# Kernel optimization log

Hardware: AMD Instinct MI355X
Metric: run time of the kernel (lower is better)

## Reference

```python
import jax, jax.numpy as jnp
import numpy as np

B, S, D, H, DH = 2, 4096, 768, 12, 64
L = 2                      # encoder layers (reduced-depth longformer-base)
HW = 256                   # one-sided sliding window (attention_window = 512)
C = 2 * HW                 # query chunk size
NC = S // C                # number of chunks
KW = C + 2 * HW            # key-window length per chunk
V = 50265
SEP_ID, NSEP = 2, 32       # </s> token id; SEPs per block (fixed by construction)
G = NSEP + 1               # global tokens: <s> at pos 0 + all SEPs
NCLS = 5
EPS = 1e-5
NEG = -1e9


def layer_norm(x, gb):
    m = jnp.mean(x, -1, keepdims=True)
    v = jnp.var(x, -1, keepdims=True)
    return (x - m) * jax.lax.rsqrt(v + EPS) * gb[0] + gb[1]


def split_heads(x):  # [B,S,D] -> [B,H,S,DH]
    return x.reshape(B, S, H, DH).transpose(0, 2, 1, 3)


def window_gather(x):  # [B,H,S,DH] -> [B,H,NC,KW,DH] overlapping key windows
    xp = jnp.pad(x, ((0, 0), (0, 0), (HW, HW), (0, 0)))
    idx = (jnp.arange(NC) * C)[:, None] + jnp.arange(KW)[None, :]
    return xp[:, :, idx, :]


def longformer_attn(x, amask, gpos, wqkv, bqkv, wqkv_g, bqkv_g, wo, bo):
    q = split_heads(x @ wqkv[0] + bqkv[0]) / np.float32(np.sqrt(DH))
    k = split_heads(x @ wqkv[1] + bqkv[1])
    v = split_heads(x @ wqkv[2] + bqkv[2])

    # ----- local sliding-window scores (banded, chunked) -----
    kw = window_gather(k)
    vw = window_gather(v)
    qc = q.reshape(B, H, NC, C, DH)
    s_loc = jnp.einsum('bhncd,bhnkd->bhnck', qc, kw)  # [B,H,NC,C,KW]

    rel = jnp.arange(KW)[None, :] - jnp.arange(C)[:, None]          # [C,KW]
    band_ok = (rel >= 0) & (rel <= 2 * HW)
    key_pos = (jnp.arange(NC) * C)[:, None] + jnp.arange(KW)[None, :] - HW
    in_b = (key_pos >= 0) & (key_pos < S)                            # [NC,KW]
    amp = jnp.pad(amask, ((0, 0), (HW, HW)))
    idx = (jnp.arange(NC) * C)[:, None] + jnp.arange(KW)[None, :]
    am_w = amp[:, idx] > 0                                           # [B,NC,KW]
    mask = band_ok[None, None, None] & in_b[None, None, :, None, :] & am_w[:, None, :, None, :]
    s_loc = jnp.where(mask, s_loc, NEG).reshape(B, H, S, KW)

    # ----- scores of every query against the G global keys -----
    gidx = gpos[:, None, :, None]                                    # [B,1,G,1]
    kg = jnp.take_along_axis(k, gidx, axis=2)                        # [B,H,G,DH]
    vg = jnp.take_along_axis(v, gidx, axis=2)
    s_glob = jnp.einsum('bhsd,bhgd->bhsg', q, kg)                    # [B,H,S,G]

    probs = jax.nn.softmax(jnp.concatenate([s_glob, s_loc], -1), -1)
    pg, pl = probs[..., :G], probs[..., G:]
    ctx = jnp.einsum('bhsg,bhgd->bhsd', pg, vg)
    ctx = ctx + jnp.einsum('bhnck,bhnkd->bhncd', pl.reshape(B, H, NC, C, KW), vw).reshape(B, H, S, DH)

    # ----- global tokens attend to everything (separate projections) -----
    qg = split_heads(x @ wqkv_g[0] + bqkv_g[0]) / np.float32(np.sqrt(DH))
    kgf = split_heads(x @ wqkv_g[1] + bqkv_g[1])
    vgf = split_heads(x @ wqkv_g[2] + bqkv_g[2])
    qg = jnp.take_along_axis(qg, gidx, axis=2)                       # [B,H,G,DH]
    s_g = jnp.einsum('bhgd,bhsd->bhgs', qg, kgf)                     # [B,H,G,S]
    s_g = jnp.where(amask[:, None, None, :] > 0, s_g, NEG)
    og = jnp.einsum('bhgs,bhsd->bhgd', jax.nn.softmax(s_g, -1), vgf)

    ctx_m = ctx.transpose(0, 2, 1, 3).reshape(B, S, D)
    og_m = og.transpose(0, 2, 1, 3).reshape(B, G, D)
    ctx_m = ctx_m.at[jnp.arange(B)[:, None], gpos].set(og_m)         # replace global rows
    return ctx_m @ wo + bo


def setup_inputs() -> dict:
    key = jax.random.key(0)
    ks = jax.random.split(key, 12)
    ids = jax.random.randint(ks[0], (B, S), 5, V, dtype=jnp.int32)
    sep_positions = (jnp.arange(NSEP) + 1) * (S // NSEP) - 1         # SEP every 128 toks
    ids = ids.at[:, sep_positions].set(SEP_ID).at[:, 0].set(0)       # <s> at pos 0
    att = jnp.ones((B, S), jnp.int32)

    def nrm(k, shp):
        return jax.random.normal(k, shp, jnp.float32) * 0.02

    ln = jnp.stack([jnp.ones(D, jnp.float32), jnp.zeros(D, jnp.float32)])
    return dict(
        input_ids=ids, attention_mask=att,
        word_emb=nrm(ks[1], (V, D)), pos_emb=nrm(ks[2], (S + 2, D)),
        type_emb=nrm(ks[3], (D,)), emb_ln=ln,
        Wqkv=nrm(ks[4], (L, 3, D, D)), bqkv=jnp.zeros((L, 3, D), jnp.float32),
        Wqkv_g=nrm(ks[5], (L, 3, D, D)), bqkv_g=jnp.zeros((L, 3, D), jnp.float32),
        Wo=nrm(ks[6], (L, D, D)), bo=jnp.zeros((L, D), jnp.float32),
        ln1=jnp.broadcast_to(ln, (L, 2, D)),
        Wff1=nrm(ks[7], (L, D, 4 * D)), bff1=jnp.zeros((L, 4 * D), jnp.float32),
        Wff2=nrm(ks[8], (L, 4 * D, D)), bff2=jnp.zeros((L, D), jnp.float32),
        ln2=jnp.broadcast_to(ln, (L, 2, D)),
        cls_W=nrm(ks[9], (NCLS, D)), cls_b=jnp.zeros((NCLS,), jnp.float32),
    )


def reference(input_ids, attention_mask, word_emb, pos_emb, type_emb, emb_ln,
              Wqkv, bqkv, Wqkv_g, bqkv_g, Wo, bo, ln1, Wff1, bff1, Wff2, bff2,
              ln2, cls_W, cls_b):
    # global attention mask: pos 0 + every SEP (fixed count by construction)
    sep_pos = jnp.sort(jnp.where(input_ids == SEP_ID, jnp.arange(S)[None, :], S), -1)[:, :NSEP]
    sep_pos = sep_pos.astype(jnp.int32)
    gpos = jnp.concatenate([jnp.zeros((B, 1), jnp.int32), sep_pos], 1)  # [B,G]

    x = word_emb[input_ids] + pos_emb[jnp.arange(S) + 2][None] + type_emb
    x = layer_norm(x, emb_ln)
    for l in range(L):
        a = longformer_attn(x, attention_mask, gpos, Wqkv[l], bqkv[l],
                            Wqkv_g[l], bqkv_g[l], Wo[l], bo[l])
        x = layer_norm(x + a, ln1[l])
        f = jax.nn.gelu(x @ Wff1[l] + bff1[l], approximate=False) @ Wff2[l] + bff2[l]
        x = layer_norm(x + f, ln2[l])

    # gather SEP embeddings (row-major over batch then sentence) -> classifier
    h = jnp.take_along_axis(x, sep_pos[:, :, None], axis=1).reshape(B * NSEP, D)
    return h @ cls_W.T + cls_b
```

## Files before the change

kernel.cpp:

```cpp
#include <hip/hip_runtime.h>


#define Bb 2
#define Ss 4096
#define Dd 768
#define Hh 12
#define Gg 33
#define NSEPn 32
#define Ll 2
#define SPAD 4640
#define PADL 256
#define NCLSn 5
#define NCH 16
#define PARTF 1056
#define PSTR 72

typedef unsigned short u16;
typedef __attribute__((ext_vector_type(8))) short bv8;
typedef __attribute__((ext_vector_type(4))) short sv4;
typedef __attribute__((ext_vector_type(4))) float f32x4;

__device__ __forceinline__ float bf2f(u16 u) {
  unsigned v = ((unsigned)u) << 16;
  return __builtin_bit_cast(float, v);
}
__device__ __forceinline__ u16 f2bf(float f) {
  unsigned u = __builtin_bit_cast(unsigned, f);
  u += 0x7fffu + ((u >> 16) & 1u);
  return (u16)(u >> 16);
}
__device__ __forceinline__ void glds16(const void* g, void* l) {
  __builtin_amdgcn_global_load_lds(
      (const __attribute__((address_space(1))) void*)g,
      (__attribute__((address_space(3))) void*)l, 16, 0, 0);
}

__global__ __launch_bounds__(256)
void setup_kernel(int* __restrict__ cnt, u16* __restrict__ kpk,
                  u16* __restrict__ vtpk, const float* __restrict__ bqkv,
                  const float* __restrict__ bqkvg, float* __restrict__ biasc) {
  int tid = blockIdx.x * 256 + threadIdx.x;
  if (tid < Bb) cnt[tid] = 0;
  if (tid < Ll * 3840) {
    int l = tid / 3840, c = tid - l * 3840;
    float v = (c < 2304) ? bqkv[l * 2304 + c]
                         : bqkvg[(l * 3 + 1) * Dd + (c - 2304)];
    biasc[tid] = v;
  }
  const int PADW = SPAD - Ss;
  const int total = Bb * Hh * PADW * 64;
  for (int i = tid; i < total; i += gridDim.x * 256) {
    int bh = i / (PADW * 64);
    int rem = i - bh * (PADW * 64);
    int prow = rem >> 6, d = rem & 63;
    int row = (prow < PADL) ? prow : (Ss + prow);
    kpk[((size_t)bh * SPAD + row) * 64 + d] = 0;
    vtpk[((size_t)bh * 64 + d) * SPAD + row] = 0;
  }
}

__global__ void sep_find_kernel(const int* __restrict__ ids, int* __restrict__ cnt,
                                int* __restrict__ list) {
  int i = blockIdx.x * 256 + threadIdx.x;
  if (i >= Bb * Ss) return;
  int b = i >> 12;
  if (ids[i] == 2) {
    int idx = atomicAdd(&cnt[b], 1);
    if (idx < 64) list[b * 64 + idx] = i & (Ss - 1);
  }
}

__global__ void sep_sort_kernel(const int* __restrict__ cnt, const int* __restrict__ list,
                                int* __restrict__ gpos) {
  int b = blockIdx.x;
  int t = threadIdx.x;
  int n = cnt[b]; if (n > 64) n = 64;
  if (t < Gg) gpos[b * Gg + t] = (t == 0) ? 0 : (Ss - 1);
  __syncthreads();
  if (t < n) {
    int v = list[b * 64 + t];
    int rank = 0;
    for (int j = 0; j < n; ++j) rank += (list[b * 64 + j] < v) ? 1 : 0;
    if (rank < NSEPn) gpos[b * Gg + 1 + rank] = v;
  }
}

__global__ __launch_bounds__(256)
void wconv_kernel(const float* __restrict__ src0, u16* __restrict__ dst0,
                  int K, int N, int grp, int sstr, long unit, long WLs) {
  __shared__ float t[32][33];
  int z = blockIdx.z;
  const float* src = src0 + (size_t)((z / grp) * sstr + (z % grp)) * K * N;
  u16* dst = dst0 + (size_t)(z / grp) * WLs + (size_t)(z % grp) * unit;
  int n0 = blockIdx.x * 32, k0 = blockIdx.y * 32;
  int tx = threadIdx.x & 31, ty = threadIdx.x >> 5;
  #pragma unroll
  for (int i = 0; i < 4; ++i)
    t[ty + i * 8][tx] = src[(size_t)(k0 + ty + i * 8) * N + n0 + tx];
  __syncthreads();
  #pragma unroll
  for (int i = 0; i < 4; ++i)
    dst[(size_t)(n0 + ty + i * 8) * K + k0 + tx] = f2bf(t[tx][ty + i * 8]);
}

__global__ __launch_bounds__(256)
void embed_ln_kernel(const int* __restrict__ ids, const float* __restrict__ we,
                     const float* __restrict__ pe, const float* __restrict__ te,
                     const float* __restrict__ lnp, float* __restrict__ x,
                     u16* __restrict__ xb) {
  int row = blockIdx.x;
  int s = row & (Ss - 1);
  int id = ids[row];
  int tid = threadIdx.x;
  float v[3]; float sm = 0.f, s2 = 0.f;
  #pragma unroll
  for (int i = 0; i < 3; ++i) {
    int c = tid + i * 256;
    float t = we[(size_t)id * Dd + c] + pe[(size_t)(s + 2) * Dd + c] + te[c];
    v[i] = t; sm += t; s2 += t * t;
  }
  __shared__ float r1[256], r2[256];
  r1[tid] = sm; r2[tid] = s2; __syncthreads();
  for (int o = 128; o; o >>= 1) {
    if (tid < o) { r1[tid] += r1[tid + o]; r2[tid] += r2[tid + o]; }
    __syncthreads();
  }
  float mean = r1[0] * (1.f / 768.f);
  float var  = r2[0] * (1.f / 768.f) - mean * mean;
  float rs = rsqrtf(var + 1e-5f);
  #pragma unroll
  for (int i = 0; i < 3; ++i) {
    int c = tid + i * 256;
    float o = (v[i] - mean) * rs * lnp[c] + lnp[Dd + c];
    x[(size_t)row * Dd + c] = o;
    xb[(size_t)row * Dd + c] = f2bf(o);
  }
}

__global__ __launch_bounds__(256)
void add_ln3_kernel(const float* __restrict__ xin, const float* __restrict__ y0,
                    const u16* __restrict__ y1, const float* __restrict__ lnp,
                    float* __restrict__ xout, u16* __restrict__ xbout) {
  int row = blockIdx.x;
  int tid = threadIdx.x;
  float v[3]; float sm = 0.f, s2 = 0.f;
  #pragma unroll
  for (int i = 0; i < 3; ++i) {
    int c = tid + i * 256;
    size_t idx = (size_t)row * Dd + c;
    float t = xin[idx] + y0[idx] + bf2f(y1[idx]);
    v[i] = t; sm += t; s2 += t * t;
  }
  __shared__ float r1[256], r2[256];
  r1[tid] = sm; r2[tid] = s2; __syncthreads();
  for (int o = 128; o; o >>= 1) {
    if (tid < o) { r1[tid] += r1[tid + o]; r2[tid] += r2[tid + o]; }
    __syncthreads();
  }
  float mean = r1[0] * (1.f / 768.f);
  float var  = r2[0] * (1.f / 768.f) - mean * mean;
  float rs = rsqrtf(var + 1e-5f);
  #pragma unroll
  for (int i = 0; i < 3; ++i) {
    int c = tid + i * 256;
    float o = (v[i] - mean) * rs * lnp[c] + lnp[Dd + c];
    xout[(size_t)row * Dd + c] = o;
    xbout[(size_t)row * Dd + c] = f2bf(o);
  }
}

template <int MODE, bool XSWZ>
__global__ __launch_bounds__(256)
void gemm2_kernel(const u16* __restrict__ A, const u16* __restrict__ Bt,
                  const float* __restrict__ bias, float* __restrict__ outf,
                  u16* __restrict__ o0, u16* __restrict__ o1, u16* __restrict__ o2,
                  u16* __restrict__ o3, u16* __restrict__ o4,
                  int N, int Ks, int Kl, float scale) {
  __shared__ u16 la[2][128 * 32], lb[2][128 * 32];
  int tid = threadIdx.x;
  int wave = tid >> 6, lane = tid & 63;
  int wr = wave >> 1, wc = wave & 1;
  int lg = lane >> 4, lc = lane & 15;
  int bx = blockIdx.x, by = blockIdx.y;
  if (XSWZ) {
    int gx = gridDim.x;
    int nlin = bx + gx * by;
    int NB = gx * gridDim.y;
    nlin = (nlin & 7) * (NB >> 3) + (nlin >> 3);
    bx = nlin % gx;
    by = nlin / gx;
  }
  int row0 = by * 128, col0 = bx * 128;
  int koff = blockIdx.z * Kl;

  int sgr = (lane & 3) ^ ((lane >> 3) & 3);
  const u16* Ag = A + (size_t)(row0 + wave * 32 + (lane >> 2)) * Ks + sgr * 8 + koff;
  const u16* Bg = Bt + (size_t)(col0 + wave * 32 + (lane >> 2)) * Ks + sgr * 8 + koff;
  int wofs = wave * 1024;
  int gph = (lg ^ ((lc >> 1) & 3)) * 8;

  f32x4 acc[4][4];
  #pragma unroll
  for (int m = 0; m < 4; ++m)
    #pragma unroll
    for (int n = 0; n < 4; ++n) acc[m][n] = (f32x4){0.f, 0.f, 0.f, 0.f};

  glds16(Ag, la[0] + wofs);
  glds16(Ag + (size_t)16 * Ks, la[0] + wofs + 512);
  glds16(Bg, lb[0] + wofs);
  glds16(Bg + (size_t)16 * Ks, lb[0] + wofs + 512);
  __syncthreads();

  int nk = Kl >> 5;
  for (int t = 0; t < nk; ++t) {
    int cur = t & 1;
    if (t + 1 < nk) {
      int k1 = (t + 1) << 5;
      glds16(Ag + k1, la[cur ^ 1] + wofs);
      glds16(Ag + (size_t)16 * Ks + k1, la[cur ^ 1] + wofs + 512);
      glds16(Bg + k1, lb[cur ^ 1] + wofs);
      glds16(Bg + (size_t)16 * Ks + k1, lb[cur ^ 1] + wofs + 512);
    }
    bv8 af[4], bf_[4];
    #pragma unroll
    for (int m = 0; m < 4; ++m)
      af[m] = *reinterpret_cast<const bv8*>(la[cur] + (wr * 64 + m * 16 + lc) * 32 + gph);
    #pragma unroll
    for (int n = 0; n < 4; ++n)
      bf_[n] = *reinterpret_cast<const bv8*>(lb[cur] + (wc * 64 + n * 16 + lc) * 32 + gph);
    __builtin_amdgcn_s_setprio(1);
    #pragma unroll
    for (int m = 0; m < 4; ++m)
      #pragma unroll
      for (int n = 0; n < 4; ++n)
        acc[m][n] = __builtin_amdgcn_mfma_f32_16x16x32_bf16(af[m], bf_[n], acc[m][n], 0, 0, 0);
    __builtin_amdgcn_s_setprio(0);
    __syncthreads();
  }

  #pragma unroll
  for (int m = 0; m < 4; ++m) {
    int grow0 = row0 + wr * 64 + m * 16 + lg * 4;
    #pragma unroll
    for (int n = 0; n < 4; ++n) {
      int gcol = col0 + wc * 64 + n * 16 + lc;
      float bvl = bias[gcol];
      if (MODE == 0) {
        if (blockIdx.z == 0) {
          #pragma unroll
          for (int r = 0; r < 4; ++r)
            outf[(size_t)(grow0 + r) * N + gcol] = acc[m][n][r] + bvl;
        } else {
          #pragma unroll
          for (int r = 0; r < 4; ++r)
            o0[(size_t)(grow0 + r) * N + gcol] = f2bf(acc[m][n][r]);
        }
      } else if (MODE == 1) {
        #pragma unroll
        for (int r = 0; r < 4; ++r) {
          float v = acc[m][n][r] + bvl;
          v = 0.5f * v * (1.0f + erff(v * 0.70710678118654752f));
          o0[(size_t)(grow0 + r) * N + gcol] = f2bf(v);
        }
      } else if (MODE == 4) {
        #pragma unroll
        for (int r = 0; r < 4; ++r)
          o0[(size_t)(grow0 + r) * N + gcol] = f2bf((acc[m][n][r] + bvl) * scale);
      } else if (MODE == 2) {
        int sec = (col0 >> 7) / 6;
        int colr = gcol - sec * 768;
        int hh = colr >> 6, d = colr & 63;
        int bb = grow0 >> 12, s = grow0 & (Ss - 1);
        size_t bhh = (size_t)(bb * Hh + hh);
        if (sec == 0) {
          #pragma unroll
          for (int r = 0; r < 4; ++r)
            o0[(bhh * Ss + s + r) * 64 + d] = f2bf((acc[m][n][r] + bvl) * scale);
        } else if (sec == 1) {
          #pragma unroll
          for (int r = 0; r < 4; ++r)
            o1[(bhh * SPAD + PADL + s + r) * 64 + d] = f2bf(acc[m][n][r] + bvl);
        } else if (sec == 2) {
          sv4 pk;
          #pragma unroll
          for (int r = 0; r < 4; ++r) pk[r] = (short)f2bf(acc[m][n][r] + bvl);
          *reinterpret_cast<sv4*>(o2 + (bhh * 64 + d) * SPAD + PADL + s) = pk;
        } else if (sec == 3) {
          #pragma unroll
          for (int r = 0; r < 4; ++r)
            o3[(bhh * Ss + s + r) * 64 + d] = f2bf(acc[m][n][r] + bvl);
        } else {
          sv4 pk;
          #pragma unroll
          for (int r = 0; r < 4; ++r) pk[r] = (short)f2bf(acc[m][n][r] + bvl);
          *reinterpret_cast<sv4*>(o4 + (bhh * 64 + d) * Ss + s) = pk;
        }
      }
    }
  }
}

__global__ __launch_bounds__(256)
void gather_glob_kernel(const u16* __restrict__ kpk, const u16* __restrict__ vtpk,
                        const int* __restrict__ gpos, u16* __restrict__ kg,
                        u16* __restrict__ vgt) {
  int bh = blockIdx.x;
  int b = bh / Hh;
  int tid = threadIdx.x;
  for (int idx = tid; idx < 64 * 64; idx += 256) {
    int g = idx >> 6, d = idx & 63;
    u16 kv = 0, vv = 0;
    if (g < Gg) {
      int p = gpos[b * Gg + g];
      kv = kpk[((size_t)bh * SPAD + PADL + p) * 64 + d];
      vv = vtpk[((size_t)bh * 64 + d) * SPAD + PADL + p];
    }
    kg[(size_t)bh * 4096 + idx] = kv;
    vgt[((size_t)bh * 64 + d) * 64 + g] = vv;
  }
}

__global__ __launch_bounds__(256)
void gather_xg_kernel(const u16* __restrict__ xb, const int* __restrict__ gpos,
                      u16* __restrict__ xg) {
  int rg = blockIdx.x;
  int b = rg / Gg;
  int p = gpos[rg];
  int tid = threadIdx.x;
  for (int c = tid; c < Dd; c += 256)
    xg[(size_t)rg * Dd + c] = xb[((size_t)b * Ss + p) * Dd + c];
}

#define LOCAL_NB (Bb * Hh * (Ss / 64))
__global__ __launch_bounds__(128)
void attn_local_kernel(const u16* __restrict__ qpk, const u16* __restrict__ kpk,
                       const u16* __restrict__ vtpk, const u16* __restrict__ kg,
                       const u16* __restrict__ vgt, const int* __restrict__ amask,
                       u16* __restrict__ ctx) {
  __shared__ u16 Plds[4][16 * PSTR];
  int bid = blockIdx.x;
  int swz = (bid & 7) * (LOCAL_NB / 8) + (bid >> 3);
  int qb = swz & 63;
  int bh = swz >> 6;
  int b = bh / Hh;
  int h = bh - b * Hh;
  int wv = threadIdx.x >> 6;
  int q0 = qb * 64;
  int qA = q0 + wv * 32;
  int lane = threadIdx.x & 63;
  int lg = lane >> 4, lc = lane & 15;
  int lg4 = lg * 4;
  int qa = qA + lc, qbq = qA + 16 + lc;

  const u16* qrowA = qpk + ((size_t)bh * Ss + qA + lc) * 64;
  bv8 aqA0 = *reinterpret_cast<const bv8*>(qrowA + lg * 8);
  bv8 aqA1 = *reinterpret_cast<const bv8*>(qrowA + 32 + lg * 8);
  const u16* qrowB = qrowA + 16 * 64;
  bv8 aqB0 = *reinterpret_cast<const bv8*>(qrowB + lg * 8);
  bv8 aqB1 = *reinterpret_cast<const bv8*>(qrowB + 32 + lg * 8);

  f32x4 oA[4], oB[4];
  #pragma unroll
  for (int i = 0; i < 4; ++i) { oA[i] = (f32x4){0.f,0.f,0.f,0.f}; oB[i] = (f32x4){0.f,0.f,0.f,0.f}; }
  float mrunA = -1e30f, lrunA = 0.f, mrunB = -1e30f, lrunB = 0.f;

  const u16* kgb = kg + ((size_t)bh) * 64 * 64;
  const u16* vgb = vgt + ((size_t)bh) * 64 * 64;
  const u16* kb = kpk + ((size_t)bh) * SPAD * 64;
  const u16* vb = vtpk + ((size_t)bh) * 64 * SPAD;
  const int* amb = amask + b * Ss;
  u16* PA = &Plds[wv * 2][0];
  u16* PB = &Plds[wv * 2 + 1][0];

  bv8 kc[8];
  #pragma unroll
  for (int j = 0; j < 4; ++j) {
    const u16* kr = kgb + (size_t)(j * 16 + lc) * 64;
    kc[2 * j]     = *reinterpret_cast<const bv8*>(kr + lg * 8);
    kc[2 * j + 1] = *reinterpret_cast<const bv8*>(kr + 32 + lg * 8);
  }
  int amvN;
  { int ni = min(max(q0 - 256 + lane, 0), Ss - 1); amvN = amb[ni]; }

  for (int step = 0; step < 10; ++step) {
    bool isg = (step == 0);
    int ks = isg ? 0 : (q0 - 256 + (step - 1) * 64);
    int amvC = amvN;
    if (step < 9) { int ni = min(max(q0 - 256 + step * 64 + lane, 0), Ss - 1); amvN = amb[ni]; }

    bv8 vf0[4], vf1[4];
    #pragma unroll
    for (int nt = 0; nt < 4; ++nt) {
      const u16* vr = isg ? (vgb + (size_t)(nt * 16 + lc) * 64)
                          : (vb + (size_t)(nt * 16 + lc) * SPAD + PADL + ks);
      vf0[nt] = *reinterpret_cast<const bv8*>(vr + lg * 8);
      vf1[nt] = *reinterpret_cast<const bv8*>(vr + 32 + lg * 8);
    }
    unsigned long long kmask;
    if (isg) {
      kmask = (1ull << Gg) - 1;
    } else {
      int kidx = ks + lane;
      kmask = __ballot((kidx >= 0) && (kidx < Ss) && (amvC > 0));
    }
    f32x4 scA[4], scB[4];
    __builtin_amdgcn_s_setprio(1);
    #pragma unroll
    for (int j = 0; j < 4; ++j) {
      f32x4 z = (f32x4){0.f, 0.f, 0.f, 0.f};
      scA[j] = __builtin_amdgcn_mfma_f32_16x16x32_bf16(kc[2 * j], aqA0, z, 0, 0, 0);
      scA[j] = __builtin_amdgcn_mfma_f32_16x16x32_bf16(kc[2 * j + 1], aqA1, scA[j], 0, 0, 0);
      scB[j] = __builtin_amdgcn_mfma_f32_16x16x32_bf16(kc[2 * j], aqB0, z, 0, 0, 0);
      scB[j] = __builtin_amdgcn_mfma_f32_16x16x32_bf16(kc[2 * j + 1], aqB1, scB[j], 0, 0, 0);
    }
    __builtin_amdgcn_s_setprio(0);
    if (step < 9) {
      int ksn = q0 - 256 + step * 64;
      #pragma unroll
      for (int j = 0; j < 4; ++j) {
        const u16* kr = kb + (size_t)(PADL + ksn + j * 16 + lc) * 64;
        kc[2 * j]     = *reinterpret_cast<const bv8*>(kr + lg * 8);
        kc[2 * j + 1] = *reinterpret_cast<const bv8*>(kr + 32 + lg * 8);
      }
    }
    bool fast = (!isg) && (step >= 2) && (step <= 8) && (kmask == ~0ull);
    float mlocA = -1e30f, mlocB = -1e30f;
    if (fast) {
      #pragma unroll
      for (int j = 0; j < 4; ++j)
        #pragma unroll
        for (int r = 0; r < 4; ++r) {
          mlocA = fmaxf(mlocA, scA[j][r]);
          mlocB = fmaxf(mlocB, scB[j][r]);
        }
    } else {
      #pragma unroll
      for (int j = 0; j < 4; ++j)
        #pragma unroll
        for (int r = 0; r < 4; ++r) {
          int kk = ks + j * 16 + lg4 + r;
          bool okk = (kmask >> (j * 16 + lg4 + r)) & 1;
          bool okA = okk, okB = okk;
          if (!isg) {
            okA = okA && ((unsigned)(kk - qa + 256) <= 512u);
            okB = okB && ((unsigned)(kk - qbq + 256) <= 512u);
          }
          scA[j][r] = okA ? scA[j][r] : -1e9f;
          scB[j][r] = okB ? scB[j][r] : -1e9f;
          mlocA = fmaxf(mlocA, scA[j][r]);
          mlocB = fmaxf(mlocB, scB[j][r]);
        }
    }
    mlocA = fmaxf(mlocA, __shfl_xor(mlocA, 16));
    mlocA = fmaxf(mlocA, __shfl_xor(mlocA, 32));
    mlocB = fmaxf(mlocB, __shfl_xor(mlocB, 16));
    mlocB = fmaxf(mlocB, __shfl_xor(mlocB, 32));
    if (__any(mlocA > mrunA + 8.f)) {
      float nm = fmaxf(mrunA, mlocA);
      float scal = __expf(mrunA - nm);
      mrunA = nm;
      lrunA *= scal;
      #pragma unroll
      for (int r = 0; r < 4; ++r) {
        float sr = __shfl(scal, lg4 + r);
        #pragma unroll
        for (int nt = 0; nt < 4; ++nt) oA[nt][r] *= sr;
      }
    }
    if (__any(mlocB > mrunB + 8.f)) {
      float nm = fmaxf(mrunB, mlocB);
      float scal = __expf(mrunB - nm);
      mrunB = nm;
      lrunB *= scal;
      #pragma unroll
      for (int r = 0; r < 4; ++r) {
        float sr = __shfl(scal, lg4 + r);
        #pragma unroll
        for (int nt = 0; nt < 4; ++nt) oB[nt][r] *= sr;
      }
    }
    float psumA = 0.f, psumB = 0.f;
    #pragma unroll
    for (int j = 0; j < 4; ++j) {
      sv4 pkA, pkB;
      #pragma unroll
      for (int r = 0; r < 4; ++r) {
        float pA = __expf(scA[j][r] - mrunA);
        float pB = __expf(scB[j][r] - mrunB);
        psumA += pA; psumB += pB;
        pkA[r] = (short)f2bf(pA);
        pkB[r] = (short)f2bf(pB);
      }
      *reinterpret_cast<sv4*>(PA + lc * PSTR + j * 16 + lg4) = pkA;
      *reinterpret_cast<sv4*>(PB + lc * PSTR + j * 16 + lg4) = pkB;
    }
    psumA += __shfl_xor(psumA, 16);
    psumA += __shfl_xor(psumA, 32);
    psumB += __shfl_xor(psumB, 16);
    psumB += __shfl_xor(psumB, 32);
    lrunA += psumA;
    lrunB += psumB;
    __builtin_amdgcn_s_setprio(1);
    {
      bv8 apA = *reinterpret_cast<const bv8*>(PA + lc * PSTR + lg * 8);
      bv8 apB = *reinterpret_cast<const bv8*>(PB + lc * PSTR + lg * 8);
      #pragma unroll
      for (int nt = 0; nt < 4; ++nt) {
        oA[nt] = __builtin_amdgcn_mfma_f32_16x16x32_bf16(apA, vf0[nt], oA[nt], 0, 0, 0);
        oB[nt] = __builtin_amdgcn_mfma_f32_16x16x32_bf16(apB, vf0[nt], oB[nt], 0, 0, 0);
      }
      apA = *reinterpret_cast<const bv8*>(PA + lc * PSTR + 32 + lg * 8);
      apB = *reinterpret_cast<const bv8*>(PB + lc * PSTR + 32 + lg * 8);
      #pragma unroll
      for (int nt = 0; nt < 4; ++nt) {
        oA[nt] = __builtin_amdgcn_mfma_f32_16x16x32_bf16(apA, vf1[nt], oA[nt], 0, 0, 0);
        oB[nt] = __builtin_amdgcn_mfma_f32_16x16x32_bf16(apB, vf1[nt], oB[nt], 0, 0, 0);
      }
    }
    __builtin_amdgcn_s_setprio(0);
  }
  float invA = 1.0f / lrunA, invB = 1.0f / lrunB;
  #pragma unroll
  for (int r = 0; r < 4; ++r) {
    float invrA = __shfl(invA, lg4 + r);
    float invrB = __shfl(invB, lg4 + r);
    size_t rowA = ((size_t)b * Ss + qA + lg4 + r) * Dd + h * 64;
    size_t rowB = rowA + (size_t)16 * Dd;
    #pragma unroll
    for (int nt = 0; nt < 4; ++nt) {
      ctx[rowA + nt * 16 + lc] = f2bf(oA[nt][r] * invrA);
      ctx[rowB + nt * 16 + lc] = f2bf(oB[nt][r] * invrB);
    }
  }
}

__global__ __launch_bounds__(192)
void attn_globalq_kernel(const u16* __restrict__ qgb, const u16* __restrict__ kgf,
                         const u16* __restrict__ vgt, const int* __restrict__ amask,
                         float* __restrict__ part) {
  __shared__ u16 Plds[3][16 * PSTR];
  int blk = blockIdx.x;
  int ch = blk & (NCH - 1);
  int bh = blk / NCH;
  int b = bh / Hh, h = bh - b * Hh;
  int wv = threadIdx.x >> 6;
  int lane = threadIdx.x & 63;
  int lg = lane >> 4, lc = lane & 15;
  int lg4 = lg * 4;

  int qrow = wv * 16 + lc;
  bv8 aq0 = (bv8)0, aq1 = (bv8)0;
  if (qrow < Gg) {
    const u16* qr = qgb + (size_t)(b * Gg + qrow) * Dd + h * 64;
    aq0 = *reinterpret_cast<const bv8*>(qr + lg * 8);
    aq1 = *reinterpret_cast<const bv8*>(qr + 32 + lg * 8);
  }

  f32x4 o[4];
  #pragma unroll
  for (int i = 0; i < 4; ++i) o[i] = (f32x4){0.f, 0.f, 0.f, 0.f};
  float mrun = -1e30f, lrun = 0.f;

  const u16* kb = kgf + ((size_t)bh) * Ss * 64;
  const u16* vb = vgt + ((size_t)bh) * 64 * Ss;
  const int* amb = amask + b * Ss;
  int ks0 = ch * (Ss / NCH);
  u16* P = &Plds[wv][0];

  bv8 kc[8];
  #pragma unroll
  for (int j = 0; j < 4; ++j) {
    const u16* kr = kb + (size_t)(ks0 + j * 16 + lc) * 64;
    kc[2 * j]     = *reinterpret_cast<const bv8*>(kr + lg * 8);
    kc[2 * j + 1] = *reinterpret_cast<const bv8*>(kr + 32 + lg * 8);
  }

  for (int st = 0; st < 4; ++st) {
    int ks = ks0 + st * 64;
    bv8 vf0[4], vf1[4];
    #pragma unroll
    for (int nt = 0; nt < 4; ++nt) {
      const u16* vr = vb + (size_t)(nt * 16 + lc) * Ss + ks;
      vf0[nt] = *reinterpret_cast<const bv8*>(vr + lg * 8);
      vf1[nt] = *reinterpret_cast<const bv8*>(vr + 32 + lg * 8);
    }
    unsigned long long kmask = __ballot(amb[ks + lane] > 0);
    f32x4 sc[4];
    __builtin_amdgcn_s_setprio(1);
    #pragma unroll
    for (int j = 0; j < 4; ++j) {
      f32x4 z = (f32x4){0.f, 0.f, 0.f, 0.f};
      sc[j] = __builtin_amdgcn_mfma_f32_16x16x32_bf16(kc[2 * j], aq0, z, 0, 0, 0);
      sc[j] = __builtin_amdgcn_mfma_f32_16x16x32_bf16(kc[2 * j + 1], aq1, sc[j], 0, 0, 0);
    }
    __builtin_amdgcn_s_setprio(0);
    if (st < 3) {
      int ksn = ks0 + (st + 1) * 64;
      #pragma unroll
      for (int j = 0; j < 4; ++j) {
        const u16* kr = kb + (size_t)(ksn + j * 16 + lc) * 64;
        kc[2 * j]     = *reinterpret_cast<const bv8*>(kr + lg * 8);
        kc[2 * j + 1] = *reinterpret_cast<const bv8*>(kr + 32 + lg * 8);
      }
    }
    float mloc = -1e30f;
    if (kmask == ~0ull) {
      #pragma unroll
      for (int j = 0; j < 4; ++j)
        #pragma unroll
        for (int r = 0; r < 4; ++r) mloc = fmaxf(mloc, sc[j][r]);
    } else {
      #pragma unroll
      for (int j = 0; j < 4; ++j)
        #pragma unroll
        for (int r = 0; r < 4; ++r) {
          bool ok = (kmask >> (j * 16 + lg4 + r)) & 1;
          sc[j][r] = ok ? sc[j][r] : -1e9f;
          mloc = fmaxf(mloc, sc[j][r]);
        }
    }
    mloc = fmaxf(mloc, __shfl_xor(mloc, 16));
    mloc = fmaxf(mloc, __shfl_xor(mloc, 32));
    if (__any(mloc > mrun + 8.f)) {
      float nm = fmaxf(mrun, mloc);
      float scal = __expf(mrun - nm);
      mrun = nm;
      lrun *= scal;
      #pragma unroll
      for (int r = 0; r < 4; ++r) {
        float sr = __shfl(scal, lg4 + r);
        #pragma unroll
        for (int nt = 0; nt < 4; ++nt) o[nt][r] *= sr;
      }
    }
    float psum = 0.f;
    #pragma unroll
    for (int j = 0; j < 4; ++j) {
      sv4 pk;
      #pragma unroll
      for (int r = 0; r < 4; ++r) {
        float p = __expf(sc[j][r] - mrun);
        psum += p;
        pk[r] = (short)f2bf(p);
      }
      *reinterpret_cast<sv4*>(P + lc * PSTR + j * 16 + lg4) = pk;
    }
    psum += __shfl_xor(psum, 16);
    psum += __shfl_xor(psum, 32);
    lrun += psum;
    __builtin_amdgcn_s_setprio(1);
    {
      bv8 ap = *reinterpret_cast<const bv8*>(P + lc * PSTR + lg * 8);
      #pragma unroll
      for (int nt = 0; nt < 4; ++nt)
        o[nt] = __builtin_amdgcn_mfma_f32_16x16x32_bf16(ap, vf0[nt], o[nt], 0, 0, 0);
      ap = *reinterpret_cast<const bv8*>(P + lc * PSTR + 32 + lg * 8);
      #pragma unroll
      for (int nt = 0; nt < 4; ++nt)
        o[nt] = __builtin_amdgcn_mfma_f32_16x16x32_bf16(ap, vf1[nt], o[nt], 0, 0, 0);
    }
    __builtin_amdgcn_s_setprio(0);
  }

  float* pb = part + ((size_t)(bh * 3 + wv) * NCH + ch) * PARTF;
  #pragma unroll
  for (int r = 0; r < 4; ++r) {
    int row = lg4 + r;
    #pragma unroll
    for (int nt = 0; nt < 4; ++nt)
      pb[row * 64 + nt * 16 + lc] = o[nt][r];
  }
  if (lg == 0) {
    pb[1024 + lc] = mrun;
    pb[1040 + lc] = lrun;
  }
}

__global__ __launch_bounds__(256)
void attn_gmerge_kernel(const float* __restrict__ part, const int* __restrict__ gpos,
                        u16* __restrict__ ctx) {
  __shared__ float wgt[Gg][NCH];
  __shared__ float sinvl[Gg];
  int bh = blockIdx.x;
  int b = bh / Hh, h = bh - b * Hh;
  int tid = threadIdx.x;
  if (tid < Gg) {
    int qt = tid >> 4, rr = tid & 15;
    const float* pb = part + ((size_t)(bh * 3 + qt) * NCH) * PARTF;
    float mx = -1e30f;
    for (int c = 0; c < NCH; ++c) mx = fmaxf(mx, pb[c * PARTF + 1024 + rr]);
    float l = 0.f;
    for (int c = 0; c < NCH; ++c) {
      float w = __expf(pb[c * PARTF + 1024 + rr] - mx);
      wgt[tid][c] = w;
      l += w * pb[c * PARTF + 1040 + rr];
    }
    sinvl[tid] = 1.0f / l;
  }
  __syncthreads();
  for (int e = tid; e < Gg * 64; e += 256) {
    int row = e >> 6, d = e & 63;
    int qt = row >> 4, rr = row & 15;
    const float* pb = part + ((size_t)(bh * 3 + qt) * NCH) * PARTF + rr * 64 + d;
    float acc = 0.f;
    #pragma unroll
    for (int c = 0; c < NCH; ++c) acc += wgt[row][c] * pb[c * PARTF];
    int pos = gpos[b * Gg + row];
    ctx[((size_t)b * Ss + pos) * Dd + h * 64 + d] = f2bf(acc * sinvl[row]);
  }
}

__global__ __launch_bounds__(64)
void cls_kernel(const float* __restrict__ x, const float* __restrict__ W,
                const float* __restrict__ bias, const int* __restrict__ gpos,
                float* __restrict__ out) {
  int r = blockIdx.x;
  int b = r >> 5, i = r & 31;
  int pos = gpos[b * Gg + 1 + i];
  int lane = threadIdx.x;
  const float* xr = x + ((size_t)b * Ss + pos) * Dd;
  float acc[NCLSn] = {0.f, 0.f, 0.f, 0.f, 0.f};
  for (int k = lane; k < Dd; k += 64) {
    float xv = xr[k];
    #pragma unroll
    for (int c = 0; c < NCLSn; ++c) acc[c] += xv * W[c * Dd + k];
  }
  #pragma unroll
  for (int c = 0; c < NCLSn; ++c) {
    #pragma unroll
    for (int off = 1; off < 64; off <<= 1) acc[c] += __shfl_xor(acc[c], off);
  }
  if (lane == 0) {
    #pragma unroll
    for (int c = 0; c < NCLSn; ++c) out[r * NCLSn + c] = acc[c] + bias[c];
  }
}

extern "C" void kernel_launch(void* const* d_in, const int* in_sizes, int n_in,
                              void* d_out, int out_size, void* d_ws, size_t ws_size,
                              hipStream_t stream) {
  const int* ids     = (const int*)d_in[0];
  const int* amask   = (const int*)d_in[1];
  const float* we    = (const float*)d_in[2];
  const float* pe    = (const float*)d_in[3];
  const float* te    = (const float*)d_in[4];
  const float* embln = (const float*)d_in[5];
  const float* Wqkv  = (const float*)d_in[6];
  const float* bqkv  = (const float*)d_in[7];
  const float* Wqkvg = (const float*)d_in[8];
  const float* bqkvg = (const float*)d_in[9];
  const float* Wo    = (const float*)d_in[10];
  const float* bo    = (const float*)d_in[11];
  const float* ln1   = (const float*)d_in[12];
  const float* Wff1  = (const float*)d_in[13];
  const float* bff1  = (const float*)d_in[14];
  const float* Wff2  = (const float*)d_in[15];
  const float* bff2  = (const float*)d_in[16];
  const float* ln2   = (const float*)d_in[17];
  const float* clsW  = (const float*)d_in[18];
  const float* clsb  = (const float*)d_in[19];
  float* out = (float*)d_out;

  char* ws = (char*)d_ws;
  size_t off = 0;
  auto alloc = [&](size_t bytes) { size_t o = off; off += (bytes + 255) & ~(size_t)255; return o; };

  const size_t DD = (size_t)Dd * Dd;
  const size_t DF = (size_t)Dd * 4 * Dd;
  const size_t WL = 7 * DD + 2 * DF;

  size_t o_cnt  = alloc(Bb * 4);
  size_t o_list = alloc(Bb * 64 * 4);
  size_t o_gpos = alloc(Bb * Gg * 4);
  size_t o_bias = alloc((size_t)Ll * 3840 * 4);
  size_t o_w    = alloc(WL * Ll * 2);
  size_t o_x    = alloc((size_t)Bb * Ss * Dd * 4);
  size_t o_xb   = alloc((size_t)Bb * Ss * Dd * 2);
  size_t o_kgf  = alloc((size_t)Bb * Hh * Ss * 64 * 2);
  size_t o_vgf  = alloc((size_t)Bb * Hh * Ss * 64 * 2);
  size_t o_accB = o_kgf;
  size_t o_qpk  = alloc((size_t)Bb * Hh * Ss * 64 * 2);
  size_t o_kpk  = alloc((size_t)Bb * Hh * SPAD * 64 * 2);
  size_t o_vtpk = alloc((size_t)Bb * Hh * 64 * SPAD * 2);
  size_t o_kg   = alloc((size_t)Bb * Hh * 64 * 64 * 2);
  size_t o_vgt  = alloc((size_t)Bb * Hh * 64 * 64 * 2);
  size_t o_xg   = alloc((size_t)128 * Dd * 2);
  size_t o_qg   = alloc((size_t)128 * Dd * 2);
  size_t o_part = alloc((size_t)Bb * Hh * 3 * NCH * PARTF * 4);
  size_t o_f1b  = o_qpk;
  {
    size_t f1b_bytes = (size_t)Bb * Ss * 4 * Dd * 2;
    if (off - o_qpk < f1b_bytes) off = o_qpk + ((f1b_bytes + 255) & ~(size_t)255);
  }
  size_t o_ctx = alloc((size_t)Bb * Ss * Dd * 2);
  size_t o_acc = alloc((size_t)Bb * Ss * Dd * 4);
  if (ws_size < off) return;

  u16* Wb = (u16*)(ws + o_w);
  int* gposp = (int*)(ws + o_gpos);
  float* accA = (float*)(ws + o_acc);
  u16* accB = (u16*)(ws + o_accB);

  setup_kernel<<<512, 256, 0, stream>>>((int*)(ws + o_cnt), (u16*)(ws + o_kpk),
      (u16*)(ws + o_vtpk), bqkv, bqkvg, (float*)(ws + o_bias));

  sep_find_kernel<<<(Bb * Ss + 255) / 256, 256, 0, stream>>>(ids, (int*)(ws + o_cnt), (int*)(ws + o_list));
  sep_sort_kernel<<<Bb, 64, 0, stream>>>((int*)(ws + o_cnt), (int*)(ws + o_list), gposp);

  wconv_kernel<<<dim3(24, 24, 6), 256, 0, stream>>>(Wqkv,       Wb,          Dd, Dd, 3, 3, (long)DD, (long)WL);
  wconv_kernel<<<dim3(24, 24, 2), 256, 0, stream>>>(Wqkvg + DD,     Wb + 3 * DD, Dd, Dd, 1, 3, 0L, (long)WL);
  wconv_kernel<<<dim3(24, 24, 2), 256, 0, stream>>>(Wqkvg + 2 * DD, Wb + 4 * DD, Dd, Dd, 1, 3, 0L, (long)WL);
  wconv_kernel<<<dim3(24, 24, 2), 256, 0, stream>>>(Wqkvg,          Wb + 5 * DD, Dd, Dd, 1, 3, 0L, (long)WL);
  wconv_kernel<<<dim3(24, 24, 2), 256, 0, stream>>>(Wo,         Wb + 6 * DD, Dd, Dd, 1, 1, 0L, (long)WL);
  wconv_kernel<<<dim3(96, 24, 2), 256, 0, stream>>>(Wff1,       Wb + 7 * DD, Dd, 4 * Dd, 1, 1, 0L, (long)WL);
  wconv_kernel<<<dim3(24, 96, 2), 256, 0, stream>>>(Wff2,       Wb + 7 * DD + DF, 4 * Dd, Dd, 1, 1, 0L, (long)WL);

  embed_ln_kernel<<<Bb * Ss, 256, 0, stream>>>(ids, we, pe, te, embln, (float*)(ws + o_x), (u16*)(ws + o_xb));

  for (int l = 0; l < Ll; ++l) {
    size_t wb = (size_t)l * WL;
    u16* xb = (u16*)(ws + o_xb);
    gemm2_kernel<2, true><<<dim3(30, 64), 256, 0, stream>>>(xb, Wb + wb, (float*)(ws + o_bias) + (size_t)l * 3840,
        nullptr,
        (u16*)(ws + o_qpk), (u16*)(ws + o_kpk), (u16*)(ws + o_vtpk),
        (u16*)(ws + o_kgf), (u16*)(ws + o_vgf), 3840, Dd, Dd, 0.125f);
    gather_glob_kernel<<<Bb * Hh, 256, 0, stream>>>((u16*)(ws + o_kpk), (u16*)(ws + o_vtpk), gposp, (u16*)(ws + o_kg), (u16*)(ws + o_vgt));
    gather_xg_kernel<<<Bb * Gg, 256, 0, stream>>>(xb, gposp, (u16*)(ws + o_xg));
    gemm2_kernel<4, false><<<dim3(6, 1), 256, 0, stream>>>((u16*)(ws + o_xg), Wb + wb + 5 * DD, bqkvg + (size_t)l * 3 * Dd,
        nullptr, (u16*)(ws + o_qg), nullptr, nullptr, nullptr, nullptr, Dd, Dd, Dd, 0.125f);
    attn_local_kernel<<<LOCAL_NB, 128, 0, stream>>>((u16*)(ws + o_qpk), (u16*)(ws + o_kpk), (u16*)(ws + o_vtpk), (u16*)(ws + o_kg), (u16*)(ws + o_vgt), amask, (u16*)(ws + o_ctx));
    attn_globalq_kernel<<<Bb * Hh * NCH, 192, 0, stream>>>((u16*)(ws + o_qg), (u16*)(ws + o_kgf), (u16*)(ws + o_vgf), amask, (float*)(ws + o_part));
    attn_gmerge_kernel<<<Bb * Hh, 256, 0, stream>>>((float*)(ws + o_part), gposp, (u16*)(ws + o_ctx));
    gemm2_kernel<0, true><<<dim3(6, 64, 2), 256, 0, stream>>>((u16*)(ws + o_ctx), Wb + wb + 6 * DD, bo + (size_t)l * Dd, accA,
        accB, nullptr, nullptr, nullptr, nullptr, Dd, Dd, Dd / 2, 1.0f);
    add_ln3_kernel<<<Bb * Ss, 256, 0, stream>>>((float*)(ws + o_x), accA, accB, ln1 + (size_t)l * 2 * Dd, (float*)(ws + o_x), xb);
    gemm2_kernel<1, true><<<dim3(24, 64), 256, 0, stream>>>(xb, Wb + wb + 7 * DD, bff1 + (size_t)l * 4 * Dd, nullptr,
        (u16*)(ws + o_f1b), nullptr, nullptr, nullptr, nullptr, 4 * Dd, Dd, Dd, 1.0f);
    gemm2_kernel<0, true><<<dim3(6, 64, 2), 256, 0, stream>>>((u16*)(ws + o_f1b), Wb + wb + 7 * DD + DF, bff2 + (size_t)l * Dd, accA,
        accB, nullptr, nullptr, nullptr, nullptr, Dd, 4 * Dd, 2 * Dd, 1.0f);
    add_ln3_kernel<<<Bb * Ss, 256, 0, stream>>>((float*)(ws + o_x), accA, accB, ln2 + (size_t)l * 2 * Dd, (float*)(ws + o_x), xb);
  }

  cls_kernel<<<Bb * NSEPn, 64, 0, stream>>>((float*)(ws + o_x), clsW, clsb, gposp, out);
}
```

Baseline: 760.7 us.

## Keep residual stream in bf16 only and merge gather kernels

The fp32 residual copy of x is dropped. Embedding, add+layernorm and the split-K output GEMMs now read and write only bf16 buffers, and the fp32 accumulator buffer is replaced by a bf16 buffer aliased onto existing workspace. This cuts global memory traffic in the layernorm and GEMM epilogues. The two small global-token gather kernels are merged into one launch. In exchange, residual accumulation happens in bf16, which loses precision across layers.

```diff
diff --git a/kernel.cpp b/kernel.cpp
--- a/kernel.cpp
+++ b/kernel.cpp
@@ -106,8 +106,7 @@
 __global__ __launch_bounds__(256)
 void embed_ln_kernel(const int* __restrict__ ids, const float* __restrict__ we,
                      const float* __restrict__ pe, const float* __restrict__ te,
-                     const float* __restrict__ lnp, float* __restrict__ x,
-                     u16* __restrict__ xb) {
+                     const float* __restrict__ lnp, u16* __restrict__ xb) {
   int row = blockIdx.x;
   int s = row & (Ss - 1);
   int id = ids[row];
@@ -132,15 +131,13 @@
   for (int i = 0; i < 3; ++i) {
     int c = tid + i * 256;
     float o = (v[i] - mean) * rs * lnp[c] + lnp[Dd + c];
-    x[(size_t)row * Dd + c] = o;
     xb[(size_t)row * Dd + c] = f2bf(o);
   }
 }
 
 __global__ __launch_bounds__(256)
-void add_ln3_kernel(const float* __restrict__ xin, const float* __restrict__ y0,
-                    const u16* __restrict__ y1, const float* __restrict__ lnp,
-                    float* __restrict__ xout, u16* __restrict__ xbout) {
+void add_ln3_kernel(u16* __restrict__ xio, const u16* __restrict__ y0,
+                    const u16* __restrict__ y1, const float* __restrict__ lnp) {
   int row = blockIdx.x;
   int tid = threadIdx.x;
   float v[3]; float sm = 0.f, s2 = 0.f;
@@ -148,7 +145,7 @@
   for (int i = 0; i < 3; ++i) {
     int c = tid + i * 256;
     size_t idx = (size_t)row * Dd + c;
-    float t = xin[idx] + y0[idx] + bf2f(y1[idx]);
+    float t = bf2f(xio[idx]) + bf2f(y0[idx]) + bf2f(y1[idx]);
     v[i] = t; sm += t; s2 += t * t;
   }
   __shared__ float r1[256], r2[256];
@@ -164,15 +161,14 @@
   for (int i = 0; i < 3; ++i) {
     int c = tid + i * 256;
     float o = (v[i] - mean) * rs * lnp[c] + lnp[Dd + c];
-    xout[(size_t)row * Dd + c] = o;
-    xbout[(size_t)row * Dd + c] = f2bf(o);
+    xio[(size_t)row * Dd + c] = f2bf(o);
   }
 }
 
 template <int MODE, bool XSWZ>
 __global__ __launch_bounds__(256)
 void gemm2_kernel(const u16* __restrict__ A, const u16* __restrict__ Bt,
-                  const float* __restrict__ bias, float* __restrict__ outf,
+                  const float* __restrict__ bias,
                   u16* __restrict__ o0, u16* __restrict__ o1, u16* __restrict__ o2,
                   u16* __restrict__ o3, u16* __restrict__ o4,
                   int N, int Ks, int Kl, float scale) {
@@ -246,15 +242,11 @@
       int gcol = col0 + wc * 64 + n * 16 + lc;
       float bvl = bias[gcol];
       if (MODE == 0) {
-        if (blockIdx.z == 0) {
-          #pragma unroll
-          for (int r = 0; r < 4; ++r)
-            outf[(size_t)(grow0 + r) * N + gcol] = acc[m][n][r] + bvl;
-        } else {
-          #pragma unroll
-          for (int r = 0; r < 4; ++r)
-            o0[(size_t)(grow0 + r) * N + gcol] = f2bf(acc[m][n][r]);
-        }
+        u16* od = blockIdx.z ? o1 : o0;
+        float badd = blockIdx.z ? 0.f : bvl;
+        #pragma unroll
+        for (int r = 0; r < 4; ++r)
+          od[(size_t)(grow0 + r) * N + gcol] = f2bf(acc[m][n][r] + badd);
       } else if (MODE == 1) {
         #pragma unroll
         for (int r = 0; r < 4; ++r) {
@@ -301,34 +293,33 @@
 }
 
 __global__ __launch_bounds__(256)
-void gather_glob_kernel(const u16* __restrict__ kpk, const u16* __restrict__ vtpk,
-                        const int* __restrict__ gpos, u16* __restrict__ kg,
-                        u16* __restrict__ vgt) {
-  int bh = blockIdx.x;
-  int b = bh / Hh;
+void gather_kernel(const u16* __restrict__ kpk, const u16* __restrict__ vtpk,
+                   const u16* __restrict__ xb, const int* __restrict__ gpos,
+                   u16* __restrict__ kg, u16* __restrict__ vgt,
+                   u16* __restrict__ xg) {
+  int blk = blockIdx.x;
   int tid = threadIdx.x;
-  for (int idx = tid; idx < 64 * 64; idx += 256) {
-    int g = idx >> 6, d = idx & 63;
-    u16 kv = 0, vv = 0;
-    if (g < Gg) {
-      int p = gpos[b * Gg + g];
-      kv = kpk[((size_t)bh * SPAD + PADL + p) * 64 + d];
-      vv = vtpk[((size_t)bh * 64 + d) * SPAD + PADL + p];
-    }
-    kg[(size_t)bh * 4096 + idx] = kv;
-    vgt[((size_t)bh * 64 + d) * 64 + g] = vv;
-  }
-}
-
-__global__ __launch_bounds__(256)
-void gather_xg_kernel(const u16* __restrict__ xb, const int* __restrict__ gpos,
-                      u16* __restrict__ xg) {
-  int rg = blockIdx.x;
-  int b = rg / Gg;
-  int p = gpos[rg];
-  int tid = threadIdx.x;
-  for (int c = tid; c < Dd; c += 256)
-    xg[(size_t)rg * Dd + c] = xb[((size_t)b * Ss + p) * Dd + c];
+  if (blk < Bb * Hh) {
+    int bh = blk;
+    int b = bh / Hh;
+    for (int idx = tid; idx < 64 * 64; idx += 256) {
+      int g = idx >> 6, d = idx & 63;
+      u16 kv = 0, vv = 0;
+      if (g < Gg) {
+        int p = gpos[b * Gg + g];
+        kv = kpk[((size_t)bh * SPAD + PADL + p) * 64 + d];
+        vv = vtpk[((size_t)bh * 64 + d) * SPAD + PADL + p];
+      }
+      kg[(size_t)bh * 4096 + idx] = kv;
+      vgt[((size_t)bh * 64 + d) * 64 + g] = vv;
+    }
+  } else {
+    int rg = blk - Bb * Hh;
+    int b = rg / Gg;
+    int p = gpos[rg];
+    for (int c = tid; c < Dd; c += 256)
+      xg[(size_t)rg * Dd + c] = xb[((size_t)b * Ss + p) * Dd + c];
+  }
 }
 
 #define LOCAL_NB (Bb * Hh * (Ss / 64))
@@ -711,17 +702,17 @@
 }
 
 __global__ __launch_bounds__(64)
-void cls_kernel(const float* __restrict__ x, const float* __restrict__ W,
+void cls_kernel(const u16* __restrict__ x, const float* __restrict__ W,
                 const float* __restrict__ bias, const int* __restrict__ gpos,
                 float* __restrict__ out) {
   int r = blockIdx.x;
   int b = r >> 5, i = r & 31;
   int pos = gpos[b * Gg + 1 + i];
   int lane = threadIdx.x;
-  const float* xr = x + ((size_t)b * Ss + pos) * Dd;
+  const u16* xr = x + ((size_t)b * Ss + pos) * Dd;
   float acc[NCLSn] = {0.f, 0.f, 0.f, 0.f, 0.f};
   for (int k = lane; k < Dd; k += 64) {
-    float xv = xr[k];
+    float xv = bf2f(xr[k]);
     #pragma unroll
     for (int c = 0; c < NCLSn; ++c) acc[c] += xv * W[c * Dd + k];
   }
@@ -774,11 +765,11 @@
   size_t o_gpos = alloc(Bb * Gg * 4);
   size_t o_bias = alloc((size_t)Ll * 3840 * 4);
   size_t o_w    = alloc(WL * Ll * 2);
-  size_t o_x    = alloc((size_t)Bb * Ss * Dd * 4);
   size_t o_xb   = alloc((size_t)Bb * Ss * Dd * 2);
   size_t o_kgf  = alloc((size_t)Bb * Hh * Ss * 64 * 2);
   size_t o_vgf  = alloc((size_t)Bb * Hh * Ss * 64 * 2);
   size_t o_accB = o_kgf;
+  size_t o_accA = o_vgf;
   size_t o_qpk  = alloc((size_t)Bb * Hh * Ss * 64 * 2);
   size_t o_kpk  = alloc((size_t)Bb * Hh * SPAD * 64 * 2);
   size_t o_vtpk = alloc((size_t)Bb * Hh * 64 * SPAD * 2);
@@ -793,12 +784,12 @@
     if (off - o_qpk < f1b_bytes) off = o_qpk + ((f1b_bytes + 255) & ~(size_t)255);
   }
   size_t o_ctx = alloc((size_t)Bb * Ss * Dd * 2);
-  size_t o_acc = alloc((size_t)Bb * Ss * Dd * 4);
   if (ws_size < off) return;
 
   u16* Wb = (u16*)(ws + o_w);
   int* gposp = (int*)(ws + o_gpos);
-  float* accA = (float*)(ws + o_acc);
+  u16* xb = (u16*)(ws + o_xb);
+  u16* accA = (u16*)(ws + o_accA);
   u16* accB = (u16*)(ws + o_accB);
 
   setup_kernel<<<512, 256, 0, stream>>>((int*)(ws + o_cnt), (u16*)(ws + o_kpk),
@@ -815,31 +806,29 @@
   wconv_kernel<<<dim3(96, 24, 2), 256, 0, stream>>>(Wff1,       Wb + 7 * DD, Dd, 4 * Dd, 1, 1, 0L, (long)WL);
   wconv_kernel<<<dim3(24, 96, 2), 256, 0, stream>>>(Wff2,       Wb + 7 * DD + DF, 4 * Dd, Dd, 1, 1, 0L, (long)WL);
 
-  embed_ln_kernel<<<Bb * Ss, 256, 0, stream>>>(ids, we, pe, te, embln, (float*)(ws + o_x), (u16*)(ws + o_xb));
+  embed_ln_kernel<<<Bb * Ss, 256, 0, stream>>>(ids, we, pe, te, embln, xb);
 
   for (int l = 0; l < Ll; ++l) {
     size_t wb = (size_t)l * WL;
-    u16* xb = (u16*)(ws + o_xb);
     gemm2_kernel<2, true><<<dim3(30, 64), 256, 0, stream>>>(xb, Wb + wb, (float*)(ws + o_bias) + (size_t)l * 3840,
-        nullptr,
         (u16*)(ws + o_qpk), (u16*)(ws + o_kpk), (u16*)(ws + o_vtpk),
         (u16*)(ws + o_kgf), (u16*)(ws + o_vgf), 3840, Dd, Dd, 0.125f);
-    gather_glob_kernel<<<Bb * Hh, 256, 0, stream>>>((u16*)(ws + o_kpk), (u16*)(ws + o_vtpk), gposp, (u16*)(ws + o_kg), (u16*)(ws + o_vgt));
-    gather_xg_kernel<<<Bb * Gg, 256, 0, stream>>>(xb, gposp, (u16*)(ws + o_xg));
+    gather_kernel<<<Bb * Hh + Bb * Gg, 256, 0, stream>>>((u16*)(ws + o_kpk), (u16*)(ws + o_vtpk), xb, gposp,
+        (u16*)(ws + o_kg), (u16*)(ws + o_vgt), (u16*)(ws + o_xg));
     gemm2_kernel<4, false><<<dim3(6, 1), 256, 0, stream>>>((u16*)(ws + o_xg), Wb + wb + 5 * DD, bqkvg + (size_t)l * 3 * Dd,
-        nullptr, (u16*)(ws + o_qg), nullptr, nullptr, nullptr, nullptr, Dd, Dd, Dd, 0.125f);
+        (u16*)(ws + o_qg), nullptr, nullptr, nullptr, nullptr, Dd, Dd, Dd, 0.125f);
     attn_local_kernel<<<LOCAL_NB, 128, 0, stream>>>((u16*)(ws + o_qpk), (u16*)(ws + o_kpk), (u16*)(ws + o_vtpk), (u16*)(ws + o_kg), (u16*)(ws + o_vgt), amask, (u16*)(ws + o_ctx));
     attn_globalq_kernel<<<Bb * Hh * NCH, 192, 0, stream>>>((u16*)(ws + o_qg), (u16*)(ws + o_kgf), (u16*)(ws + o_vgf), amask, (float*)(ws + o_part));
     attn_gmerge_kernel<<<Bb * Hh, 256, 0, stream>>>((float*)(ws + o_part), gposp, (u16*)(ws + o_ctx));
-    gemm2_kernel<0, true><<<dim3(6, 64, 2), 256, 0, stream>>>((u16*)(ws + o_ctx), Wb + wb + 6 * DD, bo + (size_t)l * Dd, accA,
-        accB, nullptr, nullptr, nullptr, nullptr, Dd, Dd, Dd / 2, 1.0f);
-    add_ln3_kernel<<<Bb * Ss, 256, 0, stream>>>((float*)(ws + o_x), accA, accB, ln1 + (size_t)l * 2 * Dd, (float*)(ws + o_x), xb);
-    gemm2_kernel<1, true><<<dim3(24, 64), 256, 0, stream>>>(xb, Wb + wb + 7 * DD, bff1 + (size_t)l * 4 * Dd, nullptr,
+    gemm2_kernel<0, true><<<dim3(6, 64, 2), 256, 0, stream>>>((u16*)(ws + o_ctx), Wb + wb + 6 * DD, bo + (size_t)l * Dd,
+        accA, accB, nullptr, nullptr, nullptr, Dd, Dd, Dd / 2, 1.0f);
+    add_ln3_kernel<<<Bb * Ss, 256, 0, stream>>>(xb, accA, accB, ln1 + (size_t)l * 2 * Dd);
+    gemm2_kernel<1, true><<<dim3(24, 64), 256, 0, stream>>>(xb, Wb + wb + 7 * DD, bff1 + (size_t)l * 4 * Dd,
         (u16*)(ws + o_f1b), nullptr, nullptr, nullptr, nullptr, 4 * Dd, Dd, Dd, 1.0f);
-    gemm2_kernel<0, true><<<dim3(6, 64, 2), 256, 0, stream>>>((u16*)(ws + o_f1b), Wb + wb + 7 * DD + DF, bff2 + (size_t)l * Dd, accA,
-        accB, nullptr, nullptr, nullptr, nullptr, Dd, 4 * Dd, 2 * Dd, 1.0f);
-    add_ln3_kernel<<<Bb * Ss, 256, 0, stream>>>((float*)(ws + o_x), accA, accB, ln2 + (size_t)l * 2 * Dd, (float*)(ws + o_x), xb);
-  }
-
-  cls_kernel<<<Bb * NSEPn, 64, 0, stream>>>((float*)(ws + o_x), clsW, clsb, gposp, out);
-}
+    gemm2_kernel<0, true><<<dim3(6, 64, 2), 256, 0, stream>>>((u16*)(ws + o_f1b), Wb + wb + 7 * DD + DF, bff2 + (size_t)l * Dd,
+        accA, accB, nullptr, nullptr, nullptr, Dd, 4 * Dd, 2 * Dd, 1.0f);
+    add_ln3_kernel<<<Bb * Ss, 256, 0, stream>>>(xb, accA, accB, ln2 + (size_t)l * 2 * Dd);
+  }
+
+  cls_kernel<<<Bb * NSEPn, 64, 0, stream>>>(xb, clsW, clsb, gposp, out);
+}
```

New measurement: 715.4 us (median of 2 runs). -6.0%, faster.
